# Performance work log

Hardware: AMD Instinct MI355X
Metric: run time of the kernel (lower is better)

The kernel has to match this reference:

```python
import jax, jax.numpy as jnp
import numpy as np

B, N, D = 8, 1024, 512
H, F = 8, 2048
Dh = D // H
EPS = 1e-5
NEG = -1.0e9


def _layernorm(x, g, b):
    mu = jnp.mean(x, axis=-1, keepdims=True)
    var = jnp.mean(jnp.square(x - mu), axis=-1, keepdims=True)
    return (x - mu) * jax.lax.rsqrt(var + EPS) * g + b


def setup_inputs() -> dict:
    key = jax.random.key(0)
    ks = jax.random.split(key, 8)
    s = 0.02  # weight init scale
    return {
        "x": jax.random.normal(ks[0], (B, N, D), jnp.float32),
        "adjacency_logits": jax.random.normal(ks[1], (N, N), jnp.float32),
        "candidate_edge_mask": jax.random.randint(ks[2], (N, N), 0, 2).astype(jnp.bool_),
        "Wq": jax.random.normal(ks[3], (D, D), jnp.float32) * s,
        "Wk": jax.random.normal(ks[4], (D, D), jnp.float32) * s,
        "Wv": jax.random.normal(ks[5], (D, D), jnp.float32) * s,
        "Wo": jax.random.normal(ks[6], (D, D), jnp.float32) * s,
        "W1": jax.random.normal(jax.random.fold_in(key, 10), (F, D), jnp.float32) * s,
        "b1": jnp.zeros((F,), jnp.float32),
        "W2": jax.random.normal(jax.random.fold_in(key, 11), (D, F), jnp.float32) * s,
        "b2": jnp.zeros((D,), jnp.float32),
        "g_ln1": jnp.ones((D,), jnp.float32),
        "beta_ln1": jnp.zeros((D,), jnp.float32),
        "g_ln2": jnp.ones((D,), jnp.float32),
        "beta_ln2": jnp.zeros((D,), jnp.float32),
    }


def reference(x, adjacency_logits, candidate_edge_mask, Wq, Wk, Wv, Wo,
              W1, b1, W2, b2, g_ln1, beta_ln1, g_ln2, beta_ln2):
    b, n, d = x.shape
    # projections: torch Linear is x @ W^T  -> [B,H,N,Dh]
    def proj(W):
        return jnp.einsum('bnd,ed->bne', x, W).reshape(b, n, H, Dh).transpose(0, 2, 1, 3)
    q, k, v = proj(Wq), proj(Wk), proj(Wv)
    scale = 1.0 / jnp.sqrt(jnp.float32(Dh))
    scores = jnp.einsum('bhqd,bhkd->bhqk', q, k) * scale
    scores = scores + adjacency_logits[None, None]
    mask = candidate_edge_mask[None, None]  # [1,1,N,N]
    scores = jnp.where(mask, scores, NEG)
    attn = jax.nn.softmax(scores, axis=-1)
    attn = jnp.where(mask, attn, 0.0)
    ctx = jnp.einsum('bhqk,bhkd->bhqd', attn, v)
    ctx = ctx.transpose(0, 2, 1, 3).reshape(b, n, d)
    attn_out = jnp.einsum('bnd,ed->bne', ctx, Wo)
    z = _layernorm(x + attn_out, g_ln1, beta_ln1)
    h = jax.nn.relu(jnp.einsum('bnd,fd->bnf', z, W1) + b1)
    z_ffn = jnp.einsum('bnf,df->bnd', h, W2) + b2
    out = _layernorm(z + z_ffn, g_ln2, beta_ln2)
    return out, attn.mean(axis=1)
```

## Files before the change

kernel.cpp:

```cpp
#include <hip/hip_runtime.h>
#include <math.h>
#include <stdint.h>


using bf16_t = __bf16;
typedef __attribute__((__ext_vector_type__(8))) __bf16 bf16x8;
typedef __attribute__((__ext_vector_type__(4))) __bf16 bf16x4;
typedef __attribute__((__ext_vector_type__(4))) float  f32x4;

#define DEVI __device__ __forceinline__

DEVI f32x4 mfma16(bf16x8 a, bf16x8 b, f32x4 c) {
  return __builtin_amdgcn_mfma_f32_16x16x32_bf16(a, b, c, 0, 0, 0);
}

DEVI void gload_lds16(const void* g, void* l) {
  __builtin_amdgcn_global_load_lds(
      (const __attribute__((address_space(1))) uint32_t*)g,
      (__attribute__((address_space(3))) uint32_t*)l, 16, 0, 0);
}

#define NEGC  (-1.0e9f)
#define EPSC  (1e-5f)

__global__ __launch_bounds__(256) void k_cvt(const float* __restrict__ in,
                                             bf16_t* __restrict__ out, int n4) {
  int i = blockIdx.x * 256 + threadIdx.x;
  if (i < n4) {
    float4 v = ((const float4*)in)[i];
    bf16x4 o = { (__bf16)v.x, (__bf16)v.y, (__bf16)v.z, (__bf16)v.w };
    ((bf16x4*)out)[i] = o;
  }
}

__global__ __launch_bounds__(256) void k_cvtw(const float* __restrict__ wq,
                                              const float* __restrict__ wk,
                                              const float* __restrict__ wv,
                                              const float* __restrict__ wo,
                                              const float* __restrict__ w1,
                                              const float* __restrict__ w2,
                                              bf16_t* __restrict__ owq,
                                              bf16_t* __restrict__ owk,
                                              bf16_t* __restrict__ owv,
                                              bf16_t* __restrict__ owo,
                                              bf16_t* __restrict__ ow1,
                                              bf16_t* __restrict__ ow2) {
  int blk = blockIdx.x;
  const float* src; bf16_t* dst; int base;
  if      (blk < 256)  { src = wq; dst = owq; base = blk; }
  else if (blk < 512)  { src = wk; dst = owk; base = blk - 256; }
  else if (blk < 768)  { src = wv; dst = owv; base = blk - 512; }
  else if (blk < 1024) { src = wo; dst = owo; base = blk - 768; }
  else if (blk < 2048) { src = w1; dst = ow1; base = blk - 1024; }
  else                 { src = w2; dst = ow2; base = blk - 2048; }
  int i = base * 256 + threadIdx.x;
  float4 v = ((const float4*)src)[i];
  bf16x4 o = { (__bf16)v.x, (__bf16)v.y, (__bf16)v.z, (__bf16)v.w };
  ((bf16x4*)dst)[i] = o;
}

__global__ __launch_bounds__(256) void k_prep(const float* __restrict__ adj,
                                              const int* __restrict__ msk,
                                              float* __restrict__ adjm,
                                              float* __restrict__ rowmax) {
  int row  = blockIdx.x * 4 + (threadIdx.x >> 6);
  int lane = threadIdx.x & 63;
  float m = -INFINITY;
  for (int i = 0; i < 16; i++) {
    int c = lane + 64 * i;
    size_t idx = (size_t)row * 1024 + c;
    float a = adj[idx];
    bool valid = (msk[idx] != 0);
    adjm[idx] = valid ? a : NEGC;
    if (valid) m = fmaxf(m, a);
  }
  for (int off = 1; off < 64; off <<= 1) m = fmaxf(m, __shfl_xor(m, off));
  if (lane == 0) rowmax[row] = m;
}

template<int EPI>
__global__ __launch_bounds__(256) void k_gemm(const bf16_t* __restrict__ A,
                                              const bf16_t* __restrict__ B,
                                              int K, int nbx,
                                              const float* __restrict__ bias,
                                              bf16_t* __restrict__ outb,
                                              float* __restrict__ outf,
                                              int out_ncols) {
  __shared__ bf16_t lA[2][4096];
  __shared__ bf16_t lB[2][4096];
  int bid = blockIdx.x;
  int nb = bid % nbx, mb = bid / nbx;
  int tid = threadIdx.x, wid = tid >> 6, lane = tid & 63;
  int l16 = lane & 15, g = lane >> 4;
  int wr = wid >> 1, wc = wid & 1;
  int rowbase = mb * 128, c0 = nb * 128;

  int dA0 = wid * 2048 + lane * 16;
  int rA0 = dA0 >> 6;
  int cbA = ((dA0 >> 4) & 3) ^ (rA0 & 3);
  const bf16_t* Asrc0 = A + (size_t)(rowbase + rA0) * K + cbA * 8;
  const bf16_t* Asrc1 = A + (size_t)(rowbase + rA0 + 16) * K + cbA * 8;
  const bf16_t* Bsrc0 = B + (size_t)(c0 + rA0) * K + cbA * 8;
  const bf16_t* Bsrc1 = B + (size_t)(c0 + rA0 + 16) * K + cbA * 8;

  f32x4 acc[4][4];
#pragma unroll
  for (int m = 0; m < 4; m++)
#pragma unroll
    for (int n = 0; n < 4; n++) acc[m][n] = (f32x4){0.f, 0.f, 0.f, 0.f};

  gload_lds16(Asrc0, (char*)&lA[0][0] + wid * 2048);
  gload_lds16(Asrc1, (char*)&lA[0][0] + wid * 2048 + 1024);
  gload_lds16(Bsrc0, (char*)&lB[0][0] + wid * 2048);
  gload_lds16(Bsrc1, (char*)&lB[0][0] + wid * 2048 + 1024);
  __syncthreads();

  for (int k0 = 0; k0 < K; k0 += 32) {
    int buf = (k0 >> 5) & 1;
    if (k0 + 32 < K) {
      gload_lds16(Asrc0 + k0 + 32, (char*)&lA[buf ^ 1][0] + wid * 2048);
      gload_lds16(Asrc1 + k0 + 32, (char*)&lA[buf ^ 1][0] + wid * 2048 + 1024);
      gload_lds16(Bsrc0 + k0 + 32, (char*)&lB[buf ^ 1][0] + wid * 2048);
      gload_lds16(Bsrc1 + k0 + 32, (char*)&lB[buf ^ 1][0] + wid * 2048 + 1024);
    }
    const char* cA = (const char*)&lA[buf][0];
    const char* cB = (const char*)&lB[buf][0];
    bf16x8 af[4], bq[4];
#pragma unroll
    for (int m = 0; m < 4; m++) {
      int row = wr * 64 + m * 16 + l16;
      af[m] = *(const bf16x8*)(cA + row * 64 + ((g ^ (row & 3)) << 4));
    }
#pragma unroll
    for (int n = 0; n < 4; n++) {
      int row = wc * 64 + n * 16 + l16;
      bq[n] = *(const bf16x8*)(cB + row * 64 + ((g ^ (row & 3)) << 4));
    }
#pragma unroll
    for (int m = 0; m < 4; m++)
#pragma unroll
      for (int n = 0; n < 4; n++) acc[m][n] = mfma16(af[m], bq[n], acc[m][n]);
    __syncthreads();
  }

  int which = c0 / out_ncols;
  int cloc0 = c0 - which * out_ncols;
  size_t obase = (size_t)which * 8192 * out_ncols;
  float osc = (EPI == 0 && which == 0) ? 0.125f : 1.0f;
#pragma unroll
  for (int n = 0; n < 4; n++) {
    int col = cloc0 + wc * 64 + n * 16 + l16;
    float bv = (EPI >= 1 && bias) ? bias[col] : 0.f;
#pragma unroll
    for (int m = 0; m < 4; m++)
#pragma unroll
      for (int j = 0; j < 4; j++) {
        int row = rowbase + wr * 64 + m * 16 + g * 4 + j;
        float v = acc[m][n][j] + bv;
        size_t idx = obase + (size_t)row * out_ncols + col;
        if (EPI == 1) outb[idx] = (__bf16)fmaxf(v, 0.f);
        else if (EPI == 0) outb[idx] = (__bf16)(v * osc);
        else outf[idx] = v;
      }
  }
}

__global__ __launch_bounds__(256) void k_resln(const float* __restrict__ gin,
                                               const float* __restrict__ residf,
                                               const bf16_t* __restrict__ residb,
                                               const float* __restrict__ gam,
                                               const float* __restrict__ bet,
                                               float* __restrict__ outf,
                                               bf16_t* __restrict__ outb) {
  int row = blockIdx.x * 4 + (threadIdx.x >> 6);
  int lane = threadIdx.x & 63;
  const float* gp = gin + (size_t)row * 512;
  float4 a0 = ((const float4*)gp)[lane];
  float4 a1 = ((const float4*)gp)[lane + 64];
  if (residf) {
    const float* rp = residf + (size_t)row * 512;
    float4 r0 = ((const float4*)rp)[lane];
    float4 r1 = ((const float4*)rp)[lane + 64];
    a0.x += r0.x; a0.y += r0.y; a0.z += r0.z; a0.w += r0.w;
    a1.x += r1.x; a1.y += r1.y; a1.z += r1.z; a1.w += r1.w;
  } else {
    const bf16_t* rp = residb + (size_t)row * 512;
    bf16x4 r0 = ((const bf16x4*)rp)[lane];
    bf16x4 r1 = ((const bf16x4*)rp)[lane + 64];
    a0.x += (float)r0[0]; a0.y += (float)r0[1]; a0.z += (float)r0[2]; a0.w += (float)r0[3];
    a1.x += (float)r1[0]; a1.y += (float)r1[1]; a1.z += (float)r1[2]; a1.w += (float)r1[3];
  }
  float s = a0.x + a0.y + a0.z + a0.w + a1.x + a1.y + a1.z + a1.w;
  for (int off = 1; off < 64; off <<= 1) s += __shfl_xor(s, off);
  float mu = s * (1.f / 512.f);
  float sq = (a0.x - mu) * (a0.x - mu) + (a0.y - mu) * (a0.y - mu) +
             (a0.z - mu) * (a0.z - mu) + (a0.w - mu) * (a0.w - mu) +
             (a1.x - mu) * (a1.x - mu) + (a1.y - mu) * (a1.y - mu) +
             (a1.z - mu) * (a1.z - mu) + (a1.w - mu) * (a1.w - mu);
  for (int off = 1; off < 64; off <<= 1) sq += __shfl_xor(sq, off);
  float rs = rsqrtf(sq * (1.f / 512.f) + EPSC);

  float4 g0 = ((const float4*)gam)[lane], g1v = ((const float4*)gam)[lane + 64];
  float4 b0 = ((const float4*)bet)[lane], b1v = ((const float4*)bet)[lane + 64];
  float4 o0, o1;
  o0.x = (a0.x - mu) * rs * g0.x + b0.x;  o0.y = (a0.y - mu) * rs * g0.y + b0.y;
  o0.z = (a0.z - mu) * rs * g0.z + b0.z;  o0.w = (a0.w - mu) * rs * g0.w + b0.w;
  o1.x = (a1.x - mu) * rs * g1v.x + b1v.x; o1.y = (a1.y - mu) * rs * g1v.y + b1v.y;
  o1.z = (a1.z - mu) * rs * g1v.z + b1v.z; o1.w = (a1.w - mu) * rs * g1v.w + b1v.w;
  if (outf) {
    float* op = outf + (size_t)row * 512;
    ((float4*)op)[lane] = o0;
    ((float4*)op)[lane + 64] = o1;
  }
  if (outb) {
    bf16_t* op = outb + (size_t)row * 512;
    bf16x4 q0 = { (__bf16)o0.x, (__bf16)o0.y, (__bf16)o0.z, (__bf16)o0.w };
    bf16x4 q1 = { (__bf16)o1.x, (__bf16)o1.y, (__bf16)o1.z, (__bf16)o1.w };
    ((bf16x4*)op)[lane] = q0;
    ((bf16x4*)op)[lane + 64] = q1;
  }
}

__global__ __launch_bounds__(256) void k_vtrans(const bf16_t* __restrict__ v,
                                                bf16_t* __restrict__ vT) {
  int bid = blockIdx.x;
  int nt = bid & 15, h = (bid >> 4) & 7, b = bid >> 7;
  __shared__ bf16_t t[64 * 66];
  int tid = threadIdx.x, wid = tid >> 6, lane = tid & 63;
  for (int i = 0; i < 16; i++) {
    int n = wid * 16 + i;
    t[lane * 66 + n] = v[(size_t)(b * 1024 + nt * 64 + n) * 512 + h * 64 + lane];
  }
  __syncthreads();
  for (int i = 0; i < 16; i++) {
    int d = wid * 16 + i;
    vT[(size_t)((b * 8 + h) * 64 + d) * 1024 + nt * 64 + lane] = t[d * 66 + lane];
  }
}

__global__ __launch_bounds__(256) void k_knorm(const bf16_t* __restrict__ kk,
                                               float* __restrict__ kmax) {
  int bh = blockIdx.x;
  int b = bh >> 3, h = bh & 7;
  int tid = threadIdx.x;
  float mx = 0.f;
  for (int n = tid; n < 1024; n += 256) {
    const bf16_t* kp = kk + (size_t)(b * 1024 + n) * 512 + h * 64;
    float ss = 0.f;
#pragma unroll
    for (int vv = 0; vv < 8; vv++) {
      bf16x8 kv = *(const bf16x8*)(kp + vv * 8);
#pragma unroll
      for (int e = 0; e < 8; e++) { float f = (float)kv[e]; ss += f * f; }
    }
    mx = fmaxf(mx, ss);
  }
  for (int off = 1; off < 64; off <<= 1) mx = fmaxf(mx, __shfl_xor(mx, off));
  __shared__ float red[4];
  if ((tid & 63) == 0) red[tid >> 6] = mx;
  __syncthreads();
  if (tid == 0) kmax[bh] = sqrtf(fmaxf(fmaxf(red[0], red[1]), fmaxf(red[2], red[3])));
}

__global__ __launch_bounds__(256) void k_cbound(const bf16_t* __restrict__ q,
                                                const float* __restrict__ kmax,
                                                const float* __restrict__ rowmax,
                                                float* __restrict__ Cb) {
  int t = blockIdx.x * 256 + threadIdx.x;
  int b = t >> 13, h = (t >> 10) & 7, n = t & 1023;
  const bf16_t* qp = q + (size_t)(b * 1024 + n) * 512 + h * 64;
  float ss = 0.f;
#pragma unroll
  for (int vv = 0; vv < 8; vv++) {
    bf16x8 kv = *(const bf16x8*)(qp + vv * 8);
#pragma unroll
    for (int e = 0; e < 8; e++) { float f = (float)kv[e]; ss += f * f; }
  }
  float am = rowmax[n];
  Cb[t] = (am < -1e30f) ? 0.f : (sqrtf(ss) * kmax[b * 8 + h] + am);
}

__global__ __launch_bounds__(256) void k_attn_ctx(const bf16_t* __restrict__ q,
                                                  const bf16_t* __restrict__ kk,
                                                  const bf16_t* __restrict__ vT,
                                                  const float* __restrict__ adjm,
                                                  const float* __restrict__ Cb,
                                                  float* __restrict__ lp,
                                                  bf16_t* __restrict__ ctxp0,
                                                  bf16_t* __restrict__ ctxp1) {
  __shared__ bf16_t ldsK[2][4096];
  __shared__ bf16_t ldsV[2][4096];
  __shared__ bf16_t pt[4][16 * 72];
  int bid = blockIdx.x;
  int split = bid & 1, qt = (bid >> 1) & 15, h = (bid >> 5) & 7, b = bid >> 8;
  int tid = threadIdx.x, wid = tid >> 6, lane = tid & 63;
  int l16 = lane & 15, g = lane >> 4;
  int qg0 = qt * 64 + wid * 16;
  bf16_t* ctxp = split ? ctxp1 : ctxp0;
  int kvbase = (b * 8 + h) * 64;

  int d0 = wid * 2048 + lane * 16;
  int row0 = d0 >> 7, row1 = (d0 + 1024) >> 7;
  int cb0 = ((d0 >> 4) & 7) ^ (row0 & 7);
  int cb1 = ((d0 >> 4) & 7) ^ (row1 & 7);
  const bf16_t* ksrc = kk + (size_t)(b * 1024) * 512 + h * 64;
  const bf16_t* vsrc = vT + (size_t)kvbase * 1024;

  auto stage = [&](int buf, int kc0) {
    gload_lds16(ksrc + (size_t)(kc0 + row0) * 512 + cb0 * 8, &ldsK[buf][wid * 1024]);
    gload_lds16(ksrc + (size_t)(kc0 + row1) * 512 + cb1 * 8, &ldsK[buf][wid * 1024 + 512]);
    gload_lds16(vsrc + (size_t)row0 * 1024 + kc0 + cb0 * 8, &ldsV[buf][wid * 1024]);
    gload_lds16(vsrc + (size_t)row1 * 1024 + kc0 + cb1 * 8, &ldsV[buf][wid * 1024 + 512]);
  };

  const bf16_t* qp = q + (size_t)(b * 1024 + qg0 + l16) * 512 + h * 64 + 8 * g;
  bf16x8 aq0 = *(const bf16x8*)qp;
  bf16x8 aq1 = *(const bf16x8*)(qp + 32);

  float Cj[4];
#pragma unroll
  for (int j = 0; j < 4; j++) Cj[j] = Cb[(b * 8 + h) * 1024 + qg0 + g * 4 + j];

  f32x4 cacc[4];
#pragma unroll
  for (int d = 0; d < 4; d++) cacc[d] = (f32x4){0.f, 0.f, 0.f, 0.f};
  float ls[4] = {0.f, 0.f, 0.f, 0.f};
  bf16_t* myp = pt[wid];
  int rph = l16 & 7;

  int ktS = split * 8, ktE = ktS + 8;
  stage(0, ktS * 64);
  __syncthreads();

  for (int kt = ktS; kt < ktE; ++kt) {
    int buf = (kt - ktS) & 1;
    int kc0 = kt * 64;
    int ktn = (kt + 1 < ktE) ? kt + 1 : kt;
    stage(buf ^ 1, ktn * 64);

    float am[4][4];
#pragma unroll
    for (int cg = 0; cg < 4; cg++)
#pragma unroll
      for (int j = 0; j < 4; j++)
        am[cg][j] = adjm[(size_t)(qg0 + g * 4 + j) * 1024 + kc0 + cg * 16 + l16];

    const char* curK = (const char*)ldsK[buf];
    const char* curV = (const char*)ldsV[buf];

#pragma unroll
    for (int cg = 0; cg < 4; cg++) {
      const char* krow = curK + ((cg * 16 + l16) << 7);
      bf16x8 k0 = *(const bf16x8*)(krow + ((g ^ rph) << 4));
      bf16x8 k1 = *(const bf16x8*)(krow + (((g + 4) ^ rph) << 4));
      f32x4 s = (f32x4){0.f, 0.f, 0.f, 0.f};
      s = mfma16(aq0, k0, s);
      s = mfma16(aq1, k1, s);
#pragma unroll
      for (int j = 0; j < 4; j++) {
        float sv = s[j] + am[cg][j];
        float p = __expf(sv - Cj[j]);
        ls[j] += p;
        myp[(g * 4 + j) * 72 + cg * 16 + l16] = (__bf16)p;
      }
    }
#pragma unroll
    for (int half = 0; half < 2; half++) {
      bf16x8 pa = *(const bf16x8*)(myp + l16 * 72 + half * 32 + 8 * g);
#pragma unroll
      for (int dg = 0; dg < 4; dg++) {
        const char* vrow = curV + ((dg * 16 + l16) << 7);
        bf16x8 vv = *(const bf16x8*)(vrow + (((g + half * 4) ^ rph) << 4));
        cacc[dg] = mfma16(pa, vv, cacc[dg]);
      }
    }
    __syncthreads();
  }

#pragma unroll
  for (int j = 0; j < 4; j++)
    for (int off = 1; off < 16; off <<= 1) ls[j] += __shfl_xor(ls[j], off);

#pragma unroll
  for (int dg = 0; dg < 4; dg++)
#pragma unroll
    for (int j = 0; j < 4; j++) {
      int row = qg0 + g * 4 + j;
      ctxp[(size_t)(b * 1024 + row) * 512 + h * 64 + dg * 16 + l16] = (__bf16)cacc[dg][j];
    }
  if (l16 == 0) {
#pragma unroll
    for (int j = 0; j < 4; j++)
      lp[split * 65536 + (b * 8 + h) * 1024 + qg0 + g * 4 + j] = ls[j];
  }
}

__global__ __launch_bounds__(256) void k_attn_fin(const bf16_t* __restrict__ ctxp0,
                                                  const bf16_t* __restrict__ ctxp1,
                                                  const float* __restrict__ lp,
                                                  const float* __restrict__ Cb,
                                                  bf16_t* __restrict__ ctx,
                                                  float* __restrict__ crl) {
  int t = blockIdx.x * 256 + threadIdx.x;
  int col4 = t & 127, row = t >> 7;
  int b = row >> 10, qq = row & 1023, h = col4 >> 4;
  int li = (b * 8 + h) * 1024 + qq;
  float l = lp[li] + lp[65536 + li];
  float rc = (l > 0.f) ? (1.f / l) : 0.f;
  bf16x4 p0 = ((const bf16x4*)ctxp0)[t];
  bf16x4 p1 = ((const bf16x4*)ctxp1)[t];
  bf16x4 o;
#pragma unroll
  for (int i = 0; i < 4; i++) o[i] = (__bf16)(((float)p0[i] + (float)p1[i]) * rc);
  ((bf16x4*)ctx)[t] = o;
  if ((col4 & 15) == 0)
    crl[li] = (l > 0.f) ? (Cb[li] + __logf(l)) : 1.0e30f;
}

__global__ __launch_bounds__(256, 4) void k_attn_mean(const bf16_t* __restrict__ q,
                                                      const bf16_t* __restrict__ kk,
                                                      const float* __restrict__ adjm,
                                                      const float* __restrict__ crl,
                                                      float* __restrict__ mout) {
  __shared__ bf16_t lds[4][2][2048];
  int bid = blockIdx.x;
  int kq = bid & 7, qt = (bid >> 3) & 15, b = bid >> 7;
  int tid = threadIdx.x, wid = tid >> 6, lane = tid & 63;
  int l16 = lane & 15, g = lane >> 4;
  int qg0 = qt * 64 + wid * 16;
  int kbase = kq * 128;
  int rl = lane >> 3;
  int cb = (lane & 7) ^ rl;
  const bf16_t* ksrc = kk + (size_t)(b * 1024 + kbase) * 512;

  auto stage = [&](int t) {
    int h = t >> 2, c = t & 3;
    char* dst = (char*)&lds[wid][t & 1][0];
    const bf16_t* sp = ksrc + (size_t)(c * 32 + rl) * 512 + h * 64 + cb * 8;
#pragma unroll
    for (int i = 0; i < 4; i++)
      gload_lds16(sp + (size_t)i * 8 * 512, dst + i * 1024);
  };

  f32x4 macc[8];
#pragma unroll
  for (int kg = 0; kg < 8; kg++) macc[kg] = (f32x4){0.f, 0.f, 0.f, 0.f};

  stage(0);

  for (int h = 0; h < 8; h++) {
    const bf16_t* qp = q + (size_t)(b * 1024 + qg0 + l16) * 512 + h * 64 + 8 * g;
    bf16x8 aq0 = *(const bf16x8*)qp;
    bf16x8 aq1 = *(const bf16x8*)(qp + 32);
    f32x4 CR = *(const f32x4*)(crl + (b * 8 + h) * 1024 + qg0 + g * 4);
#pragma unroll
    for (int c = 0; c < 4; c++) {
      int t = h * 4 + c;
      __builtin_amdgcn_sched_barrier(0);
      if (t < 31) {
        stage(t + 1);
        __builtin_amdgcn_sched_barrier(0);
        asm volatile("s_waitcnt vmcnt(4)" ::: "memory");
      } else {
        asm volatile("s_waitcnt vmcnt(0)" ::: "memory");
      }
      __builtin_amdgcn_sched_barrier(0);
      const char* cK = (const char*)&lds[wid][t & 1][0];
#pragma unroll
      for (int cg = 0; cg < 2; cg++) {
        const char* krow = cK + ((cg * 16 + l16) << 7);
        bf16x8 k0 = *(const bf16x8*)(krow + ((g ^ (l16 & 7)) << 4));
        bf16x8 k1 = *(const bf16x8*)(krow + (((g + 4) ^ (l16 & 7)) << 4));
        f32x4 s = (f32x4){0.f, 0.f, 0.f, 0.f};
        s = mfma16(aq0, k0, s);
        s = mfma16(aq1, k1, s);
        int kg = c * 2 + cg;
#pragma unroll
        for (int j = 0; j < 4; j++)
          macc[kg][j] += __expf(s[j] - CR[j]);
      }
    }
  }

#pragma unroll
  for (int kg = 0; kg < 8; kg++)
#pragma unroll
    for (int j = 0; j < 4; j++) {
      size_t off = (size_t)(qg0 + g * 4 + j) * 1024 + kbase + kg * 16 + l16;
      mout[(size_t)b * 1048576 + off] = macc[kg][j] * __expf(adjm[off]) * 0.125f;
    }
}

extern "C" void kernel_launch(void* const* d_in, const int* in_sizes, int n_in,
                              void* d_out, int out_size, void* d_ws, size_t ws_size,
                              hipStream_t stream) {
  (void)in_sizes; (void)n_in; (void)out_size; (void)ws_size;
  const float* x   = (const float*)d_in[0];
  const float* adj = (const float*)d_in[1];
  const int*   msk = (const int*)d_in[2];
  const float* Wq  = (const float*)d_in[3];
  const float* Wk  = (const float*)d_in[4];
  const float* Wv  = (const float*)d_in[5];
  const float* Wo  = (const float*)d_in[6];
  const float* W1  = (const float*)d_in[7];
  const float* b1  = (const float*)d_in[8];
  const float* W2  = (const float*)d_in[9];
  const float* b2  = (const float*)d_in[10];
  const float* g1  = (const float*)d_in[11];
  const float* be1 = (const float*)d_in[12];
  const float* g2  = (const float*)d_in[13];
  const float* be2 = (const float*)d_in[14];

  float* out  = (float*)d_out;
  float* mout = out + (size_t)8 * 1024 * 512;

  char* ws = (char*)d_ws;
  const size_t MB = 1024 * 1024;
  bf16_t* wqb = (bf16_t*)(ws);
  bf16_t* wkb = (bf16_t*)(ws + 512 * 1024);
  bf16_t* wvb = (bf16_t*)(ws + 1 * MB);
  bf16_t* wob = (bf16_t*)(ws + 3 * MB / 2);
  bf16_t* w1b = (bf16_t*)(ws + 2 * MB);
  bf16_t* w2b = (bf16_t*)(ws + 4 * MB);
  float*  Cb   = (float*)(ws + 6 * MB);
  float*  crl  = (float*)(ws + 6 * MB + 256 * 1024);
  float*  amax = (float*)(ws + 6 * MB + 512 * 1024);
  float*  kmax = (float*)(ws + 6 * MB + 768 * 1024);
  float*  lp   = (float*)(ws + 7 * MB);
  bf16_t* xb   = (bf16_t*)(ws + 8 * MB);
  bf16_t* ctx  = xb;
  bf16_t* zb   = xb;
  bf16_t* qb   = (bf16_t*)(ws + 16 * MB);
  bf16_t* kb   = (bf16_t*)(ws + 24 * MB);
  bf16_t* vb   = (bf16_t*)(ws + 32 * MB);
  bf16_t* ctxp1 = vb;
  bf16_t* vT   = (bf16_t*)(ws + 40 * MB);
  bf16_t* ctxp0 = (bf16_t*)(ws + 48 * MB);
  float*  gout1 = (float*)(ws + 16 * MB);
  bf16_t* hb    = (bf16_t*)(ws + 16 * MB);
  float*  gout2 = (float*)(ws + 48 * MB);
  float*  adjm  = (float*)(ws + 72 * MB);

  k_cvt<<<4096, 256, 0, stream>>>(x, xb, 1048576);
  k_cvtw<<<3072, 256, 0, stream>>>(Wq, Wk, Wv, Wo, W1, W2,
                                   wqb, wkb, wvb, wob, w1b, w2b);

  k_prep<<<256, 256, 0, stream>>>(adj, msk, adjm, amax);

  k_gemm<0><<<64 * 12, 256, 0, stream>>>(xb, wqb, 512, 12, nullptr, qb, nullptr, 512);
  k_vtrans<<<1024, 256, 0, stream>>>(vb, vT);
  k_knorm<<<64, 256, 0, stream>>>(kb, kmax);
  k_cbound<<<256, 256, 0, stream>>>(qb, kmax, amax, Cb);

  k_attn_ctx<<<2048, 256, 0, stream>>>(qb, kb, vT, adjm, Cb, lp, ctxp0, ctxp1);
  k_attn_fin<<<4096, 256, 0, stream>>>(ctxp0, ctxp1, lp, Cb, ctx, crl);
  k_attn_mean<<<1024, 256, 0, stream>>>(qb, kb, adjm, crl, mout);

  k_gemm<2><<<64 * 4, 256, 0, stream>>>(ctx, wob, 512, 4, nullptr, nullptr, gout1, 512);
  k_resln<<<2048, 256, 0, stream>>>(gout1, x, nullptr, g1, be1, nullptr, zb);
  k_gemm<1><<<64 * 16, 256, 0, stream>>>(zb, w1b, 512, 16, b1, hb, nullptr, 2048);
  k_gemm<2><<<64 * 4, 256, 0, stream>>>(hb, w2b, 2048, 4, b2, nullptr, gout2, 512);
  k_resln<<<2048, 256, 0, stream>>>(gout2, nullptr, zb, g2, be2, out, nullptr);
}
```

Baseline: 244.3 us.

## Precompute masked exp(adjacency) in bf16 and drop split-K attention with finalize kernel

Replaces the masked fp32 adjacency plus row-max bound with a precomputed bf16 table of exp(adj) (zero where masked), so attention multiplies by that factor instead of adding a logit before exp. Attention is no longer split into two key halves, which removes the separate finalize kernel and the partial ctx/sum buffers; normalisation and the log-sum are done in-kernel. It also prefetches the adjacency factors one tile ahead and raises wave priority around the MFMAs. The risks are halving the grid to 1024 blocks, which lowers parallelism, possible overflow or precision loss from exp(adj) in bf16 without the max shift, and a smaller stability margin in the bound.

Result: no change. 246.5 us (+0.9%).

```diff
diff --git a/kernel.cpp b/kernel.cpp
--- a/kernel.cpp
+++ b/kernel.cpp
@@ -20,7 +20,6 @@
       (__attribute__((address_space(3))) uint32_t*)l, 16, 0, 0);
 }
 
-#define NEGC  (-1.0e9f)
 #define EPSC  (1e-5f)
 
 __global__ __launch_bounds__(256) void k_cvt(const float* __restrict__ in,
@@ -61,21 +60,16 @@
 
 __global__ __launch_bounds__(256) void k_prep(const float* __restrict__ adj,
                                               const int* __restrict__ msk,
-                                              float* __restrict__ adjm,
-                                              float* __restrict__ rowmax) {
+                                              bf16_t* __restrict__ eadj) {
   int row  = blockIdx.x * 4 + (threadIdx.x >> 6);
   int lane = threadIdx.x & 63;
-  float m = -INFINITY;
   for (int i = 0; i < 16; i++) {
     int c = lane + 64 * i;
     size_t idx = (size_t)row * 1024 + c;
     float a = adj[idx];
     bool valid = (msk[idx] != 0);
-    adjm[idx] = valid ? a : NEGC;
-    if (valid) m = fmaxf(m, a);
-  }
-  for (int off = 1; off < 64; off <<= 1) m = fmaxf(m, __shfl_xor(m, off));
-  if (lane == 0) rowmax[row] = m;
+    eadj[idx] = valid ? (__bf16)__expf(a) : (__bf16)0.f;
+  }
 }
 
 template<int EPI>
@@ -264,11 +258,11 @@
 
 __global__ __launch_bounds__(256) void k_cbound(const bf16_t* __restrict__ q,
                                                 const float* __restrict__ kmax,
-                                                const float* __restrict__ rowmax,
                                                 float* __restrict__ Cb) {
   int t = blockIdx.x * 256 + threadIdx.x;
-  int b = t >> 13, h = (t >> 10) & 7, n = t & 1023;
-  const bf16_t* qp = q + (size_t)(b * 1024 + n) * 512 + h * 64;
+  int b = t >> 13, h = (t >> 10) & 7;
+  int n = t & 1023; (void)n;
+  const bf16_t* qp = q + (size_t)(b * 1024 + (t & 1023)) * 512 + h * 64;
   float ss = 0.f;
 #pragma unroll
   for (int vv = 0; vv < 8; vv++) {
@@ -276,27 +270,24 @@
 #pragma unroll
     for (int e = 0; e < 8; e++) { float f = (float)kv[e]; ss += f * f; }
   }
-  float am = rowmax[n];
-  Cb[t] = (am < -1e30f) ? 0.f : (sqrtf(ss) * kmax[b * 8 + h] + am);
+  Cb[t] = sqrtf(ss) * kmax[b * 8 + h];
 }
 
 __global__ __launch_bounds__(256) void k_attn_ctx(const bf16_t* __restrict__ q,
                                                   const bf16_t* __restrict__ kk,
                                                   const bf16_t* __restrict__ vT,
-                                                  const float* __restrict__ adjm,
+                                                  const bf16_t* __restrict__ eadj,
                                                   const float* __restrict__ Cb,
-                                                  float* __restrict__ lp,
-                                                  bf16_t* __restrict__ ctxp0,
-                                                  bf16_t* __restrict__ ctxp1) {
+                                                  bf16_t* __restrict__ ctx,
+                                                  float* __restrict__ crl) {
   __shared__ bf16_t ldsK[2][4096];
   __shared__ bf16_t ldsV[2][4096];
   __shared__ bf16_t pt[4][16 * 72];
   int bid = blockIdx.x;
-  int split = bid & 1, qt = (bid >> 1) & 15, h = (bid >> 5) & 7, b = bid >> 8;
+  int qt = bid & 15, h = (bid >> 4) & 7, b = bid >> 7;
   int tid = threadIdx.x, wid = tid >> 6, lane = tid & 63;
   int l16 = lane & 15, g = lane >> 4;
   int qg0 = qt * 64 + wid * 16;
-  bf16_t* ctxp = split ? ctxp1 : ctxp0;
   int kvbase = (b * 8 + h) * 64;
 
   int d0 = wid * 2048 + lane * 16;
@@ -327,23 +318,25 @@
   float ls[4] = {0.f, 0.f, 0.f, 0.f};
   bf16_t* myp = pt[wid];
   int rph = l16 & 7;
-
-  int ktS = split * 8, ktE = ktS + 8;
-  stage(0, ktS * 64);
+  const bf16_t* erow = eadj + (size_t)(qg0 + g * 4) * 1024 + l16;
+
+  bf16_t eaA[4][4], eaB[4][4];
+  stage(0, 0);
+#pragma unroll
+  for (int cg = 0; cg < 4; cg++)
+#pragma unroll
+    for (int j = 0; j < 4; j++) eaA[cg][j] = erow[(size_t)j * 1024 + cg * 16];
   __syncthreads();
 
-  for (int kt = ktS; kt < ktE; ++kt) {
-    int buf = (kt - ktS) & 1;
+  auto tile = [&](int kt, int buf, bf16_t (&eaC)[4][4], bf16_t (&eaN)[4][4]) {
     int kc0 = kt * 64;
-    int ktn = (kt + 1 < ktE) ? kt + 1 : kt;
+    int ktn = (kt + 1 < 16) ? kt + 1 : 15;
     stage(buf ^ 1, ktn * 64);
-
-    float am[4][4];
 #pragma unroll
     for (int cg = 0; cg < 4; cg++)
 #pragma unroll
       for (int j = 0; j < 4; j++)
-        am[cg][j] = adjm[(size_t)(qg0 + g * 4 + j) * 1024 + kc0 + cg * 16 + l16];
+        eaN[cg][j] = erow[(size_t)j * 1024 + ktn * 64 + cg * 16];
 
     const char* curK = (const char*)ldsK[buf];
     const char* curV = (const char*)ldsV[buf];
@@ -354,12 +347,13 @@
       bf16x8 k0 = *(const bf16x8*)(krow + ((g ^ rph) << 4));
       bf16x8 k1 = *(const bf16x8*)(krow + (((g + 4) ^ rph) << 4));
       f32x4 s = (f32x4){0.f, 0.f, 0.f, 0.f};
+      __builtin_amdgcn_s_setprio(1);
       s = mfma16(aq0, k0, s);
       s = mfma16(aq1, k1, s);
+      __builtin_amdgcn_s_setprio(0);
 #pragma unroll
       for (int j = 0; j < 4; j++) {
-        float sv = s[j] + am[cg][j];
-        float p = __expf(sv - Cj[j]);
+        float p = (float)eaC[cg][j] * __expf(s[j] - Cj[j]);
         ls[j] += p;
         myp[(g * 4 + j) * 72 + cg * 16 + l16] = (__bf16)p;
       }
@@ -367,59 +361,50 @@
 #pragma unroll
     for (int half = 0; half < 2; half++) {
       bf16x8 pa = *(const bf16x8*)(myp + l16 * 72 + half * 32 + 8 * g);
+      __builtin_amdgcn_s_setprio(1);
 #pragma unroll
       for (int dg = 0; dg < 4; dg++) {
         const char* vrow = curV + ((dg * 16 + l16) << 7);
         bf16x8 vv = *(const bf16x8*)(vrow + (((g + half * 4) ^ rph) << 4));
         cacc[dg] = mfma16(pa, vv, cacc[dg]);
       }
+      __builtin_amdgcn_s_setprio(0);
     }
     __syncthreads();
+  };
+
+  for (int k2 = 0; k2 < 8; k2++) {
+    tile(2 * k2,     0, eaA, eaB);
+    tile(2 * k2 + 1, 1, eaB, eaA);
   }
 
 #pragma unroll
   for (int j = 0; j < 4; j++)
     for (int off = 1; off < 16; off <<= 1) ls[j] += __shfl_xor(ls[j], off);
+  float rc[4];
+#pragma unroll
+  for (int j = 0; j < 4; j++) rc[j] = (ls[j] > 0.f) ? (1.f / ls[j]) : 0.f;
 
 #pragma unroll
   for (int dg = 0; dg < 4; dg++)
 #pragma unroll
     for (int j = 0; j < 4; j++) {
       int row = qg0 + g * 4 + j;
-      ctxp[(size_t)(b * 1024 + row) * 512 + h * 64 + dg * 16 + l16] = (__bf16)cacc[dg][j];
+      ctx[(size_t)(b * 1024 + row) * 512 + h * 64 + dg * 16 + l16] =
+          (__bf16)(cacc[dg][j] * rc[j]);
     }
   if (l16 == 0) {
 #pragma unroll
-    for (int j = 0; j < 4; j++)
-      lp[split * 65536 + (b * 8 + h) * 1024 + qg0 + g * 4 + j] = ls[j];
-  }
-}
-
-__global__ __launch_bounds__(256) void k_attn_fin(const bf16_t* __restrict__ ctxp0,
-                                                  const bf16_t* __restrict__ ctxp1,
-                                                  const float* __restrict__ lp,
-                                                  const float* __restrict__ Cb,
-                                                  bf16_t* __restrict__ ctx,
-                                                  float* __restrict__ crl) {
-  int t = blockIdx.x * 256 + threadIdx.x;
-  int col4 = t & 127, row = t >> 7;
-  int b = row >> 10, qq = row & 1023, h = col4 >> 4;
-  int li = (b * 8 + h) * 1024 + qq;
-  float l = lp[li] + lp[65536 + li];
-  float rc = (l > 0.f) ? (1.f / l) : 0.f;
-  bf16x4 p0 = ((const bf16x4*)ctxp0)[t];
-  bf16x4 p1 = ((const bf16x4*)ctxp1)[t];
-  bf16x4 o;
-#pragma unroll
-  for (int i = 0; i < 4; i++) o[i] = (__bf16)(((float)p0[i] + (float)p1[i]) * rc);
-  ((bf16x4*)ctx)[t] = o;
-  if ((col4 & 15) == 0)
-    crl[li] = (l > 0.f) ? (Cb[li] + __logf(l)) : 1.0e30f;
+    for (int j = 0; j < 4; j++) {
+      int li = (b * 8 + h) * 1024 + qg0 + g * 4 + j;
+      crl[li] = (ls[j] > 0.f) ? (Cj[j] + __logf(ls[j])) : 1.0e30f;
+    }
+  }
 }
 
 __global__ __launch_bounds__(256, 4) void k_attn_mean(const bf16_t* __restrict__ q,
                                                       const bf16_t* __restrict__ kk,
-                                                      const float* __restrict__ adjm,
+                                                      const bf16_t* __restrict__ eadj,
                                                       const float* __restrict__ crl,
                                                       float* __restrict__ mout) {
   __shared__ bf16_t lds[4][2][2048];
@@ -487,7 +472,7 @@
 #pragma unroll
     for (int j = 0; j < 4; j++) {
       size_t off = (size_t)(qg0 + g * 4 + j) * 1024 + kbase + kg * 16 + l16;
-      mout[(size_t)b * 1048576 + off] = macc[kg][j] * __expf(adjm[off]) * 0.125f;
+      mout[(size_t)b * 1048576 + off] = macc[kg][j] * (float)eadj[off] * 0.125f;
     }
 }
 
@@ -524,37 +509,32 @@
   bf16_t* w2b = (bf16_t*)(ws + 4 * MB);
   float*  Cb   = (float*)(ws + 6 * MB);
   float*  crl  = (float*)(ws + 6 * MB + 256 * 1024);
-  float*  amax = (float*)(ws + 6 * MB + 512 * 1024);
   float*  kmax = (float*)(ws + 6 * MB + 768 * 1024);
-  float*  lp   = (float*)(ws + 7 * MB);
   bf16_t* xb   = (bf16_t*)(ws + 8 * MB);
   bf16_t* ctx  = xb;
   bf16_t* zb   = xb;
   bf16_t* qb   = (bf16_t*)(ws + 16 * MB);
   bf16_t* kb   = (bf16_t*)(ws + 24 * MB);
   bf16_t* vb   = (bf16_t*)(ws + 32 * MB);
-  bf16_t* ctxp1 = vb;
   bf16_t* vT   = (bf16_t*)(ws + 40 * MB);
-  bf16_t* ctxp0 = (bf16_t*)(ws + 48 * MB);
   float*  gout1 = (float*)(ws + 16 * MB);
   bf16_t* hb    = (bf16_t*)(ws + 16 * MB);
   float*  gout2 = (float*)(ws + 48 * MB);
-  float*  adjm  = (float*)(ws + 72 * MB);
+  bf16_t* eadj  = (bf16_t*)(ws + 72 * MB);
 
   k_cvt<<<4096, 256, 0, stream>>>(x, xb, 1048576);
   k_cvtw<<<3072, 256, 0, stream>>>(Wq, Wk, Wv, Wo, W1, W2,
                                    wqb, wkb, wvb, wob, w1b, w2b);
 
-  k_prep<<<256, 256, 0, stream>>>(adj, msk, adjm, amax);
+  k_prep<<<256, 256, 0, stream>>>(adj, msk, eadj);
 
   k_gemm<0><<<64 * 12, 256, 0, stream>>>(xb, wqb, 512, 12, nullptr, qb, nullptr, 512);
   k_vtrans<<<1024, 256, 0, stream>>>(vb, vT);
   k_knorm<<<64, 256, 0, stream>>>(kb, kmax);
-  k_cbound<<<256, 256, 0, stream>>>(qb, kmax, amax, Cb);
-
-  k_attn_ctx<<<2048, 256, 0, stream>>>(qb, kb, vT, adjm, Cb, lp, ctxp0, ctxp1);
-  k_attn_fin<<<4096, 256, 0, stream>>>(ctxp0, ctxp1, lp, Cb, ctx, crl);
-  k_attn_mean<<<1024, 256, 0, stream>>>(qb, kb, adjm, crl, mout);
+  k_cbound<<<256, 256, 0, stream>>>(qb, kmax, Cb);
+
+  k_attn_ctx<<<1024, 256, 0, stream>>>(qb, kb, vT, eadj, Cb, ctx, crl);
+  k_attn_mean<<<1024, 256, 0, stream>>>(qb, kb, eadj, crl, mout);
 
   k_gemm<2><<<64 * 4, 256, 0, stream>>>(ctx, wob, 512, 4, nullptr, nullptr, gout1, 512);
   k_resln<<<2048, 256, 0, stream>>>(gout1, x, nullptr, g1, be1, nullptr, zb);
```
